# Performance work log

Hardware: AMD Instinct MI355X
Metric: run time of the kernel (lower is better)

## Reference

```python
import jax, jax.numpy as jnp
import numpy as np

N = 131072      # total nodes
B = 512         # number of graphs
F_DIM = 512     # in_channels
H = F_DIM // 2  # score_net hidden
RATIO = 0.5
MARGIN = 0.5
TOPK_LOSS_WEIGHT = 0.2


def setup_inputs() -> dict:
    key = jax.random.key(0)
    k1, k2, k3 = jax.random.split(key, 3)
    x = jax.random.normal(k1, (N, F_DIM), dtype=jnp.float32)
    # sorted segment ids: equal-sized graphs of N // B nodes
    batch = (jnp.arange(N) // (N // B)).astype(jnp.int32)
    W1 = jax.random.normal(k2, (F_DIM, H), dtype=jnp.float32) / np.sqrt(F_DIM).astype(np.float32)
    b1 = jnp.zeros((H,), dtype=jnp.float32)
    W2 = jax.random.normal(k3, (H, 1), dtype=jnp.float32) / np.sqrt(H).astype(np.float32)
    b2 = jnp.zeros((1,), dtype=jnp.float32)
    return {"x": x, "batch": batch, "W1": W1, "b1": b1, "W2": W2, "b2": b2}


def reference(x, batch, W1, b1, W2, b2):
    # scores = score_net(x).squeeze(-1)   [N]
    scores = (jax.nn.relu(x @ W1 + b1) @ W2 + b2)[:, 0]

    # per-graph node counts and k = max(1, int(ratio * n_i))
    counts = jax.ops.segment_sum(jnp.ones((N,), dtype=scores.dtype), batch, num_segments=B)
    k = jnp.maximum(1, jnp.floor(RATIO * counts).astype(jnp.int32))  # [B]

    # segmented top-k via lexsort: sort by (batch asc, score desc)
    order = jnp.lexsort((-scores, batch))          # [N] permutation
    b_sorted = batch[order]
    starts = jnp.cumsum(counts) - counts           # exclusive-cumsum segment starts
    rank = jnp.arange(N, dtype=counts.dtype) - starts[b_sorted]  # rank within graph (0 = highest score)
    sel_sorted = rank < k[b_sorted].astype(counts.dtype)
    selected_mask = jnp.zeros((N,), dtype=bool).at[order].set(sel_sorted)

    # global_add_pool over selected nodes
    m = selected_mask.astype(x.dtype)
    x_pooled = jax.ops.segment_sum(x * m[:, None], batch, num_segments=B)  # [B, F]

    # margin regularization loss per graph
    sel_cnt = jax.ops.segment_sum(m, batch, num_segments=B)
    sel_sum = jax.ops.segment_sum(scores * m, batch, num_segments=B)
    tot_sum = jax.ops.segment_sum(scores, batch, num_segments=B)
    uns_cnt = counts - sel_cnt
    sel_mean = sel_sum / jnp.maximum(sel_cnt, 1.0)
    uns_mean = (tot_sum - sel_sum) / jnp.maximum(uns_cnt, 1.0)
    per_graph = jnp.where(uns_cnt > 0, jax.nn.relu(MARGIN - (sel_mean - uns_mean)), 0.0)
    topk_loss = per_graph.sum() / B * TOPK_LOSS_WEIGHT

    return x_pooled, topk_loss, selected_mask
```

## Files before the change

kernel.cpp:

```cpp
#include <hip/hip_runtime.h>

#define BGRAPHS 512
#define FDIM    512
#define HDIM    256
#define NPG     256
#define KSEL    128
#define STAGES  16
#define BSTAGE_SHORTS 16384
#define A_ROW   40
#define A_PLANE (NPG * A_ROW)

typedef __attribute__((ext_vector_type(8)))  _Float16 f16x8;
typedef __attribute__((ext_vector_type(8)))  short    s16x8;
typedef __attribute__((ext_vector_type(16))) float    f32x16;

__device__ __forceinline__ unsigned short f16_rne(float f, float* back) {
    _Float16 h = (_Float16)f;
    *back = (float)h;
    union { _Float16 h; unsigned short s; } cv; cv.h = h;
    return cv.s;
}

__global__ __launch_bounds__(256)
void split_w1_kernel(const float* __restrict__ W1, unsigned short* __restrict__ wsB)
{
    const int uid  = blockIdx.x * 256 + threadIdx.x;
    const int lane = uid & 63;
    int t = uid >> 6;
    const int nt = t & 7;  t >>= 3;
    const int p  = t & 1;  t >>= 1;
    const int q  = t & 1;
    const int s  = t >> 1;
    const int n  = nt * 32 + (lane & 31);
    const int k0 = s * 32 + q * 16 + (lane >> 5) * 8;

    s16x8 v;
    #pragma unroll
    for (int j = 0; j < 8; ++j) {
        float w = W1[(size_t)(k0 + j) * HDIM + n] * 1024.0f;
        float f1, f2;
        unsigned short h1 = f16_rne(w, &f1);
        unsigned short h2 = f16_rne(w - f1, &f2);
        v[j] = (short)(p ? h2 : h1);
    }
    *(s16x8*)(wsB + (size_t)uid * 8) = v;
}

__global__ __launch_bounds__(512, 2)
void fused_kernel(const float* __restrict__ x,
                  const unsigned short* __restrict__ wsB,
                  const float* __restrict__ b1, const float* __restrict__ W2,
                  const float* __restrict__ b2,
                  float* __restrict__ pooled, float* __restrict__ mask_out,
                  float* __restrict__ loss_per_g)
{
    __shared__ __attribute__((aligned(16))) unsigned char smem[147456];

    const int g    = blockIdx.x;
    const int tid  = threadIdx.x;
    const int lane = tid & 63;
    const int wv   = tid >> 6;
    const int wy   = wv & 3;
    const int wx   = wv >> 2;
    const int l31  = lane & 31;
    const int lh   = lane >> 5;

    const int r  = tid >> 1;
    const int hf = tid & 1;
    const float* aptr = x + ((size_t)(g * NPG + r)) * FDIM + hf * 16;

    f32x16 acc[2][4];
    #pragma unroll
    for (int a = 0; a < 2; ++a)
        #pragma unroll
        for (int b = 0; b < 4; ++b)
            #pragma unroll
            for (int rr = 0; rr < 16; ++rr) acc[a][b][rr] = 0.f;

    float4 aA0, aA1, aA2, aA3;
    float4 aB0, aB1, aB2, aB3;

#define GLL_B(S1) do {                                                          \
    const unsigned short* _src = wsB + (size_t)(S1) * BSTAGE_SHORTS;            \
    unsigned short* _dst = (unsigned short*)smem + ((S1) & 1) * BSTAGE_SHORTS;  \
    _Pragma("unroll")                                                           \
    for (int _i = 0; _i < 4; ++_i) {                                            \
        const int _u = _i * 512 + tid;                                          \
        __builtin_amdgcn_global_load_lds(                                       \
            (const __attribute__((address_space(1))) unsigned int*)(_src + (size_t)_u * 8), \
            (__attribute__((address_space(3))) unsigned int*)(_dst + _u * 8),   \
            16, 0, 0);                                                          \
    } } while (0)

#define LOAD_PF(P0,P1,P2,P3,S2) do {                                            \
    const float* _ap = aptr + (S2) * 32;                                        \
    P0 = *(const float4*)(_ap + 0);  P1 = *(const float4*)(_ap + 4);            \
    P2 = *(const float4*)(_ap + 8);  P3 = *(const float4*)(_ap + 12); } while (0)

#define CONVERT_A(P0,P1,P2,P3,BUF) do {                                         \
    float _v[16] = {P0.x,P0.y,P0.z,P0.w,P1.x,P1.y,P1.z,P1.w,                    \
                    P2.x,P2.y,P2.z,P2.w,P3.x,P3.y,P3.z,P3.w};                   \
    unsigned short _H[16], _M[16];                                              \
    _Pragma("unroll")                                                           \
    for (int _j = 0; _j < 16; ++_j) {                                           \
        float _f1, _f2;                                                         \
        float _xs = _v[_j] * 64.0f;                            \
        _H[_j] = f16_rne(_xs, &_f1);                                            \
        _M[_j] = f16_rne(_xs - _f1, &_f2);                                      \
        (void)_f2;                                                              \
    }                                                                           \
    unsigned short* _pl = (unsigned short*)(smem + 65536 + (BUF) * 40960)       \
                          + r * A_ROW + hf * 16;                                \
    uint4 _u0, _u1;                                                             \
    _u0.x = (unsigned)_H[0]  | ((unsigned)_H[1]  << 16);                        \
    _u0.y = (unsigned)_H[2]  | ((unsigned)_H[3]  << 16);                        \
    _u0.z = (unsigned)_H[4]  | ((unsigned)_H[5]  << 16);                        \
    _u0.w = (unsigned)_H[6]  | ((unsigned)_H[7]  << 16);                        \
    _u1.x = (unsigned)_H[8]  | ((unsigned)_H[9]  << 16);                        \
    _u1.y = (unsigned)_H[10] | ((unsigned)_H[11] << 16);                        \
    _u1.z = (unsigned)_H[12] | ((unsigned)_H[13] << 16);                        \
    _u1.w = (unsigned)_H[14] | ((unsigned)_H[15] << 16);                        \
    ((uint4*)_pl)[0] = _u0; ((uint4*)_pl)[1] = _u1;                             \
    _u0.x = (unsigned)_M[0]  | ((unsigned)_M[1]  << 16);                        \
    _u0.y = (unsigned)_M[2]  | ((unsigned)_M[3]  << 16);                        \
    _u0.z = (unsigned)_M[4]  | ((unsigned)_M[5]  << 16);                        \
    _u0.w = (unsigned)_M[6]  | ((unsigned)_M[7]  << 16);                        \
    _u1.x = (unsigned)_M[8]  | ((unsigned)_M[9]  << 16);                        \
    _u1.y = (unsigned)_M[10] | ((unsigned)_M[11] << 16);                        \
    _u1.z = (unsigned)_M[12] | ((unsigned)_M[13] << 16);                        \
    _u1.w = (unsigned)_M[14] | ((unsigned)_M[15] << 16);                        \
    ((uint4*)(_pl + A_PLANE))[0] = _u0; ((uint4*)(_pl + A_PLANE))[1] = _u1;     \
    } while (0)

#define COMPUTE(BUF) do {                                                       \
    const f16x8* _bfp = (const f16x8*)(smem + (BUF) * (BSTAGE_SHORTS * 2));     \
    const unsigned short* _aB = (const unsigned short*)(smem + 65536 + (BUF) * 40960); \
    _Pragma("unroll")                                                           \
    for (int _q = 0; _q < 2; ++_q) {                                            \
        const int _a0 = (wy * 64 + l31) * A_ROW + _q * 16 + lh * 8;             \
        const int _a1 = _a0 + 32 * A_ROW;                                       \
        f16x8 A0h = *(const f16x8*)(_aB + _a0);                                 \
        f16x8 A0m = *(const f16x8*)(_aB + A_PLANE + _a0);                       \
        f16x8 A1h = *(const f16x8*)(_aB + _a1);                                 \
        f16x8 A1m = *(const f16x8*)(_aB + A_PLANE + _a1);                       \
        _Pragma("unroll")                                                       \
        for (int _nt = 0; _nt < 4; ++_nt) {                                     \
            const int _nn = wx * 4 + _nt;                                       \
            f16x8 Bh = _bfp[((_q * 2 + 0) * 8 + _nn) * 64 + lane];              \
            f16x8 Bm = _bfp[((_q * 2 + 1) * 8 + _nn) * 64 + lane];              \
            acc[0][_nt] = __builtin_amdgcn_mfma_f32_32x32x16_f16(A0h, Bh, acc[0][_nt], 0, 0, 0); \
            acc[1][_nt] = __builtin_amdgcn_mfma_f32_32x32x16_f16(A1h, Bh, acc[1][_nt], 0, 0, 0); \
            acc[0][_nt] = __builtin_amdgcn_mfma_f32_32x32x16_f16(A0m, Bh, acc[0][_nt], 0, 0, 0); \
            acc[1][_nt] = __builtin_amdgcn_mfma_f32_32x32x16_f16(A1m, Bh, acc[1][_nt], 0, 0, 0); \
            acc[0][_nt] = __builtin_amdgcn_mfma_f32_32x32x16_f16(A0h, Bm, acc[0][_nt], 0, 0, 0); \
            acc[1][_nt] = __builtin_amdgcn_mfma_f32_32x32x16_f16(A1h, Bm, acc[1][_nt], 0, 0, 0); \
            acc[0][_nt] = __builtin_amdgcn_mfma_f32_32x32x16_f16(A0m, Bm, acc[0][_nt], 0, 0, 0); \
            acc[1][_nt] = __builtin_amdgcn_mfma_f32_32x32x16_f16(A1m, Bm, acc[1][_nt], 0, 0, 0); \
        }                                                                       \
    } } while (0)

    LOAD_PF(aA0, aA1, aA2, aA3, 0);
    GLL_B(0);
    CONVERT_A(aA0, aA1, aA2, aA3, 0);
    LOAD_PF(aA0, aA1, aA2, aA3, 1);
    __syncthreads();

    for (int s = 0; s < STAGES; s += 2) {
        if (s < STAGES - 1) GLL_B(s + 1);
        if (s < STAGES - 2) LOAD_PF(aB0, aB1, aB2, aB3, s + 2);
        COMPUTE(0);
        if (s < STAGES - 1) CONVERT_A(aA0, aA1, aA2, aA3, 1);
        __syncthreads();

        if (s + 1 < STAGES - 1) GLL_B(s + 2);
        if (s + 1 < STAGES - 2) LOAD_PF(aA0, aA1, aA2, aA3, s + 3);
        COMPUTE(1);
        if (s + 1 < STAGES - 1) CONVERT_A(aB0, aB1, aB2, aB3, 0);
        __syncthreads();
    }

    float* Sp   = (float*)smem;
    float* sv   = Sp + 2 * NPG;
    int*   selr = (int*)(sv + NPG);
    float* redT = (float*)(selr + KSEL);
    float* redS = redT + NPG;

    float bb[4], ww[4];
    #pragma unroll
    for (int nt = 0; nt < 4; ++nt) {
        const int c = wx * 128 + nt * 32 + l31;
        bb[nt] = b1[c];
        ww[nt] = W2[c];
    }
    const float unscale = 1.0f / 65536.0f;
    #pragma unroll
    for (int mt = 0; mt < 2; ++mt) {
        float pr[16];
        #pragma unroll
        for (int rr = 0; rr < 16; ++rr) pr[rr] = 0.f;
        #pragma unroll
        for (int nt = 0; nt < 4; ++nt)
            #pragma unroll
            for (int rr = 0; rr < 16; ++rr) {
                float h = fmaf(acc[mt][nt][rr], unscale, bb[nt]);
                h = h > 0.f ? h : 0.f;
                pr[rr] = fmaf(h, ww[nt], pr[rr]);
            }
        #pragma unroll
        for (int mask = 1; mask <= 16; mask <<= 1)
            #pragma unroll
            for (int rr = 0; rr < 16; ++rr)
                pr[rr] += __shfl_xor(pr[rr], mask);
        if (l31 == 0) {
            #pragma unroll
            for (int rr = 0; rr < 16; ++rr) {
                const int row = wy * 64 + mt * 32 + (rr & 3) + 8 * (rr >> 2) + 4 * lh;
                Sp[wx * NPG + row] = pr[rr];
            }
        }
    }
    __syncthreads();

    float sc = 0.f;
    if (tid < NPG) {
        sc = b2[0] + Sp[tid] + Sp[NPG + tid];
        sv[tid] = sc;
    }
    __syncthreads();

    if (tid < NPG) {
        int rank = 0;
        for (int j = 0; j < NPG; ++j) {
            const float sj = sv[j];
            rank += (sj > sc || (sj == sc && j < tid)) ? 1 : 0;
        }
        const bool sel = rank < KSEL;
        mask_out[g * NPG + tid] = sel ? 1.0f : 0.0f;
        if (sel) selr[rank] = tid;
        redT[tid] = sc;
        redS[tid] = sel ? sc : 0.f;
    }
    __syncthreads();

    for (int off = 128; off > 0; off >>= 1) {
        if (tid < off) { redT[tid] += redT[tid + off]; redS[tid] += redS[tid + off]; }
        __syncthreads();
    }
    if (tid == 0) {
        const float tot = redT[0], ssum = redS[0];
        const float sel_mean = ssum * (1.0f / KSEL);
        const float uns_mean = (tot - ssum) * (1.0f / (NPG - KSEL));
        const float v = 0.5f - (sel_mean - uns_mean);
        loss_per_g[g] = v > 0.f ? v : 0.f;
    }

    const int col = tid;
    const float* __restrict__ xg = x + (size_t)g * NPG * FDIM;
    float a0 = 0.f, a1 = 0.f, a2 = 0.f, a3 = 0.f;
    #pragma unroll 4
    for (int n = 0; n < KSEL; n += 4) {
        a0 += xg[(size_t)selr[n + 0] * FDIM + col];
        a1 += xg[(size_t)selr[n + 1] * FDIM + col];
        a2 += xg[(size_t)selr[n + 2] * FDIM + col];
        a3 += xg[(size_t)selr[n + 3] * FDIM + col];
    }
    pooled[g * FDIM + col] = (a0 + a1) + (a2 + a3);

#undef GLL_B
#undef LOAD_PF
#undef CONVERT_A
#undef COMPUTE
}

__global__ __launch_bounds__(256)
void loss_kernel(const float* __restrict__ loss_per_g, float* __restrict__ out_loss)
{
    __shared__ float red[256];
    const int t = threadIdx.x;
    red[t] = loss_per_g[t] + loss_per_g[t + 256];
    __syncthreads();
    for (int off = 128; off > 0; off >>= 1) {
        if (t < off) red[t] += red[t + off];
        __syncthreads();
    }
    if (t == 0) out_loss[0] = red[0] * (0.2f / BGRAPHS);
}

extern "C" void kernel_launch(void* const* d_in, const int* in_sizes, int n_in,
                              void* d_out, int out_size, void* d_ws, size_t ws_size,
                              hipStream_t stream)
{
    const float* x  = (const float*)d_in[0];
    const float* W1 = (const float*)d_in[2];
    const float* b1 = (const float*)d_in[3];
    const float* W2 = (const float*)d_in[4];
    const float* b2 = (const float*)d_in[5];

    float* out    = (float*)d_out;
    float* pooled = out;
    float* loss   = out + BGRAPHS * FDIM;
    float* mask   = loss + 1;

    float* loss_g       = (float*)d_ws;
    unsigned short* wsB = (unsigned short*)((char*)d_ws + 4096);

    split_w1_kernel<<<128, 256, 0, stream>>>(W1, wsB);
    fused_kernel<<<BGRAPHS, 512, 0, stream>>>(x, wsB, b1, W2, b2,
                                              pooled, mask, loss_g);
    loss_kernel<<<1, 256, 0, stream>>>(loss_g, loss);
}
```

Before: 434.3 us.

## Drop low-low split-f16 MFMA terms, coalesce A loads, widen pooling accumulators

Removes the two MFMA calls that multiply the low-order f16 parts of A and B, so each K step issues six MFMAs instead of eight and the split-precision GEMM loses the smallest correction term. The x tile load now has 8 threads read contiguous float4s across a row, with each thread covering 4 rows 64 apart. This is meant to coalesce global reads better and makes the LDS stores 8 bytes per plane. The pooling loop uses 8 independent accumulators to expose more memory-level parallelism. Dropping the low-low term slightly reduces score accuracy, which could flip top-k selections near ties.

```diff
diff --git a/kernel.cpp b/kernel.cpp
--- a/kernel.cpp
+++ b/kernel.cpp
@@ -65,9 +65,9 @@
     const int l31  = lane & 31;
     const int lh   = lane >> 5;
 
-    const int r  = tid >> 1;
-    const int hf = tid & 1;
-    const float* aptr = x + ((size_t)(g * NPG + r)) * FDIM + hf * 16;
+    const int c     = tid & 7;
+    const int rbase = tid >> 3;
+    const float* aptr = x + ((size_t)(g * NPG + rbase)) * FDIM + c * 4;
 
     f32x16 acc[2][4];
     #pragma unroll
@@ -94,43 +94,36 @@
 
 #define LOAD_PF(P0,P1,P2,P3,S2) do {                                            \
     const float* _ap = aptr + (S2) * 32;                                        \
-    P0 = *(const float4*)(_ap + 0);  P1 = *(const float4*)(_ap + 4);            \
-    P2 = *(const float4*)(_ap + 8);  P3 = *(const float4*)(_ap + 12); } while (0)
-
-#define CONVERT_A(P0,P1,P2,P3,BUF) do {                                         \
-    float _v[16] = {P0.x,P0.y,P0.z,P0.w,P1.x,P1.y,P1.z,P1.w,                    \
-                    P2.x,P2.y,P2.z,P2.w,P3.x,P3.y,P3.z,P3.w};                   \
-    unsigned short _H[16], _M[16];                                              \
+    P0 = *(const float4*)(_ap + 0 * 64 * FDIM);                                 \
+    P1 = *(const float4*)(_ap + 1 * 64 * FDIM);                                 \
+    P2 = *(const float4*)(_ap + 2 * 64 * FDIM);                                 \
+    P3 = *(const float4*)(_ap + 3 * 64 * FDIM); } while (0)
+
+#define CONV1(P,KK,BUF) do {                                                    \
+    float _f[4] = {P.x, P.y, P.z, P.w};                                         \
+    unsigned short _H[4], _M[4];                                                \
     _Pragma("unroll")                                                           \
-    for (int _j = 0; _j < 16; ++_j) {                                           \
-        float _f1, _f2;                                                         \
-        float _xs = _v[_j] * 64.0f;                            \
-        _H[_j] = f16_rne(_xs, &_f1);                                            \
-        _M[_j] = f16_rne(_xs - _f1, &_f2);                                      \
-        (void)_f2;                                                              \
+    for (int _j = 0; _j < 4; ++_j) {                                            \
+        float _b1v, _b2v;                                                       \
+        float _xs = _f[_j] * 64.0f;                            \
+        _H[_j] = f16_rne(_xs, &_b1v);                                           \
+        _M[_j] = f16_rne(_xs - _b1v, &_b2v);                                    \
+        (void)_b2v;                                                             \
     }                                                                           \
     unsigned short* _pl = (unsigned short*)(smem + 65536 + (BUF) * 40960)       \
-                          + r * A_ROW + hf * 16;                                \
-    uint4 _u0, _u1;                                                             \
-    _u0.x = (unsigned)_H[0]  | ((unsigned)_H[1]  << 16);                        \
-    _u0.y = (unsigned)_H[2]  | ((unsigned)_H[3]  << 16);                        \
-    _u0.z = (unsigned)_H[4]  | ((unsigned)_H[5]  << 16);                        \
-    _u0.w = (unsigned)_H[6]  | ((unsigned)_H[7]  << 16);                        \
-    _u1.x = (unsigned)_H[8]  | ((unsigned)_H[9]  << 16);                        \
-    _u1.y = (unsigned)_H[10] | ((unsigned)_H[11] << 16);                        \
-    _u1.z = (unsigned)_H[12] | ((unsigned)_H[13] << 16);                        \
-    _u1.w = (unsigned)_H[14] | ((unsigned)_H[15] << 16);                        \
-    ((uint4*)_pl)[0] = _u0; ((uint4*)_pl)[1] = _u1;                             \
-    _u0.x = (unsigned)_M[0]  | ((unsigned)_M[1]  << 16);                        \
-    _u0.y = (unsigned)_M[2]  | ((unsigned)_M[3]  << 16);                        \
-    _u0.z = (unsigned)_M[4]  | ((unsigned)_M[5]  << 16);                        \
-    _u0.w = (unsigned)_M[6]  | ((unsigned)_M[7]  << 16);                        \
-    _u1.x = (unsigned)_M[8]  | ((unsigned)_M[9]  << 16);                        \
-    _u1.y = (unsigned)_M[10] | ((unsigned)_M[11] << 16);                        \
-    _u1.z = (unsigned)_M[12] | ((unsigned)_M[13] << 16);                        \
-    _u1.w = (unsigned)_M[14] | ((unsigned)_M[15] << 16);                        \
-    ((uint4*)(_pl + A_PLANE))[0] = _u0; ((uint4*)(_pl + A_PLANE))[1] = _u1;     \
+                          + (rbase + 64 * (KK)) * A_ROW + c * 4;                \
+    uint2 _uH, _uM;                                                             \
+    _uH.x = (unsigned)_H[0] | ((unsigned)_H[1] << 16);                          \
+    _uH.y = (unsigned)_H[2] | ((unsigned)_H[3] << 16);                          \
+    _uM.x = (unsigned)_M[0] | ((unsigned)_M[1] << 16);                          \
+    _uM.y = (unsigned)_M[2] | ((unsigned)_M[3] << 16);                          \
+    *(uint2*)_pl = _uH;                                                         \
+    *(uint2*)(_pl + A_PLANE) = _uM;                                             \
     } while (0)
+
+#define CONVERT_A(P0,P1,P2,P3,BUF) do {                                         \
+    CONV1(P0, 0, BUF); CONV1(P1, 1, BUF);                                       \
+    CONV1(P2, 2, BUF); CONV1(P3, 3, BUF); } while (0)
 
 #define COMPUTE(BUF) do {                                                       \
     const f16x8* _bfp = (const f16x8*)(smem + (BUF) * (BSTAGE_SHORTS * 2));     \
@@ -154,8 +147,6 @@
             acc[1][_nt] = __builtin_amdgcn_mfma_f32_32x32x16_f16(A1m, Bh, acc[1][_nt], 0, 0, 0); \
             acc[0][_nt] = __builtin_amdgcn_mfma_f32_32x32x16_f16(A0h, Bm, acc[0][_nt], 0, 0, 0); \
             acc[1][_nt] = __builtin_amdgcn_mfma_f32_32x32x16_f16(A1h, Bm, acc[1][_nt], 0, 0, 0); \
-            acc[0][_nt] = __builtin_amdgcn_mfma_f32_32x32x16_f16(A0m, Bm, acc[0][_nt], 0, 0, 0); \
-            acc[1][_nt] = __builtin_amdgcn_mfma_f32_32x32x16_f16(A1m, Bm, acc[1][_nt], 0, 0, 0); \
         }                                                                       \
     } } while (0)
 
@@ -188,9 +179,9 @@
     float bb[4], ww[4];
     #pragma unroll
     for (int nt = 0; nt < 4; ++nt) {
-        const int c = wx * 128 + nt * 32 + l31;
-        bb[nt] = b1[c];
-        ww[nt] = W2[c];
+        const int cc = wx * 128 + nt * 32 + l31;
+        bb[nt] = b1[cc];
+        ww[nt] = W2[cc];
     }
     const float unscale = 1.0f / 65536.0f;
     #pragma unroll
@@ -257,17 +248,23 @@
     const int col = tid;
     const float* __restrict__ xg = x + (size_t)g * NPG * FDIM;
     float a0 = 0.f, a1 = 0.f, a2 = 0.f, a3 = 0.f;
-    #pragma unroll 4
-    for (int n = 0; n < KSEL; n += 4) {
+    float a4 = 0.f, a5 = 0.f, a6 = 0.f, a7 = 0.f;
+    #pragma unroll 2
+    for (int n = 0; n < KSEL; n += 8) {
         a0 += xg[(size_t)selr[n + 0] * FDIM + col];
         a1 += xg[(size_t)selr[n + 1] * FDIM + col];
         a2 += xg[(size_t)selr[n + 2] * FDIM + col];
         a3 += xg[(size_t)selr[n + 3] * FDIM + col];
-    }
-    pooled[g * FDIM + col] = (a0 + a1) + (a2 + a3);
+        a4 += xg[(size_t)selr[n + 4] * FDIM + col];
+        a5 += xg[(size_t)selr[n + 5] * FDIM + col];
+        a6 += xg[(size_t)selr[n + 6] * FDIM + col];
+        a7 += xg[(size_t)selr[n + 7] * FDIM + col];
+    }
+    pooled[g * FDIM + col] = ((a0 + a1) + (a2 + a3)) + ((a4 + a5) + (a6 + a7));
 
 #undef GLL_B
 #undef LOAD_PF
+#undef CONV1
 #undef CONVERT_A
 #undef COMPUTE
 }
```

After: 417.3 us. -3.9%, faster.
